# Kernel optimization log

Measured on AMD Instinct MI355X. Metric: run time of the kernel, lower is better.

Reference implementation:

```python
import jax, jax.numpy as jnp
import numpy as np

B, TQ, TK, D, DV = 8, 2048, 2048, 1024, 1024  # units == TK


def setup_inputs() -> dict:
    key = jax.random.key(0)
    kq, kk, kv, kb = jax.random.split(key, 4)
    q = jax.random.normal(kq, (B, TQ, D), dtype=jnp.float32)
    k = jax.random.normal(kk, (B, D, TK), dtype=jnp.float32)
    v = jax.random.normal(kv, (B, TK, DV), dtype=jnp.float32)
    b = 0.1 * jax.random.normal(kb, (TK,), dtype=jnp.float32)  # bias over key axis (units,)
    return {"q": q, "k": k, "v": v, "b": b}


def reference(q, k, v, b):
    # scores[b,i,j] = tanh(q_i . k_j + b_j)   -- additive-style biased dot scores
    scores = jnp.tanh(jnp.einsum("bqd,bdk->bqk", q, k) + b)  # [B, TQ, TK]
    # softmax over the key axis (axis=1 of the unbatched [TQ,TK] scores)
    weights = jax.nn.softmax(scores, axis=-1)
    # weighted sum of values
    context = jnp.einsum("bqk,bkv->bqv", weights, v)  # [B, TQ, DV]
    return context
```

## Files before the change

kernel.cpp:

```cpp
#include <hip/hip_runtime.h>
#include <hip/hip_bf16.h>
#include <stdint.h>

#define B_  8
#define TQ_ 2048
#define TK_ 2048
#define D_  1024
#define DV_ 1024

typedef __attribute__((ext_vector_type(8))) short  short8;
typedef __attribute__((ext_vector_type(4))) float  floatx4;

__device__ __forceinline__ void async_copy16(const void* g, void* l) {
  __builtin_amdgcn_global_load_lds(
      (const __attribute__((address_space(1))) unsigned int*)g,
      (__attribute__((address_space(3))) unsigned int*)l,
      16, 0, 0);
}

__device__ __forceinline__ ushort f2bf(float f) {
  union { __hip_bfloat16 b; ushort u; } cv;
  cv.b = __float2bfloat16(f);
  return cv.u;
}

__device__ __forceinline__ float bf2f(ushort u) {
  union { ushort u; __hip_bfloat16 b; } cv;
  cv.u = u;
  return __bfloat162float(cv.b);
}


__global__ void cvt_bf16(const float4* __restrict__ in, ushort4* __restrict__ out, int n4) {
  int i = blockIdx.x * 256 + threadIdx.x;
  if (i < n4) {
    float4 f = in[i];
    ushort4 o;
    o.x = f2bf(f.x); o.y = f2bf(f.y); o.z = f2bf(f.z); o.w = f2bf(f.w);
    out[i] = o;
  }
}

__global__ void transpose_cvt64(const float* __restrict__ in, ushort* __restrict__ out,
                                int R, int C) {
  __shared__ float tile[64][65];
  const int t  = threadIdx.x;
  const int c0 = blockIdx.x * 64, r0 = blockIdx.y * 64;
  const size_t z = (size_t)blockIdx.z * R * C;
  {
    const int row = t >> 4, col = (t & 15) * 4;
    #pragma unroll
    for (int ro = 0; ro < 4; ro++) {
      const float4 f = *(const float4*)&in[z + (size_t)(r0 + ro * 16 + row) * C + c0 + col];
      tile[ro * 16 + row][col + 0] = f.x;
      tile[ro * 16 + row][col + 1] = f.y;
      tile[ro * 16 + row][col + 2] = f.z;
      tile[ro * 16 + row][col + 3] = f.w;
    }
  }
  __syncthreads();
  {
    const int c = t >> 4, rg = (t & 15) * 4;
    #pragma unroll
    for (int ro = 0; ro < 4; ro++) {
      const int cc = ro * 16 + c;
      ushort4 o;
      o.x = f2bf(tile[rg + 0][cc]);
      o.y = f2bf(tile[rg + 1][cc]);
      o.z = f2bf(tile[rg + 2][cc]);
      o.w = f2bf(tile[rg + 3][cc]);
      *(ushort4*)&out[z + (size_t)(c0 + cc) * R + r0 + rg] = o;
    }
  }
}

template <int KDIM>
__device__ __forceinline__ void gemm_core(const ushort* __restrict__ Ab,
                                          const ushort* __restrict__ Bb,
                                          ushort* ldsA, ushort* ldsB,
                                          int bm0, int bn0,
                                          floatx4 (&acc)[4][4]) {
  const int t    = threadIdx.x;
  const int lane = t & 63;
  const int w    = t >> 6;
  const int wm   = w >> 1, wn = w & 1;
  const int lc   = lane & 15;
  const int q    = lane >> 4;

  const int achunk = (t & 3) ^ ((t >> 3) & 3);
  const char* ga0 = (const char*)(Ab + (size_t)(bm0 + (t >> 2)) * KDIM) + achunk * 16;
  const char* ga1 = ga0 + (size_t)64 * KDIM * 2;
  const char* gb0 = (const char*)(Bb + (size_t)(bn0 + (t >> 2)) * KDIM) + achunk * 16;
  const char* gb1 = gb0 + (size_t)64 * KDIM * 2;
  char* la0 = (char*)ldsA + t * 16;
  char* la1 = (char*)ldsA + 4096 + t * 16;
  char* lb0 = (char*)ldsB + t * 16;
  char* lb1 = (char*)ldsB + 4096 + t * 16;

  const int rA = wm * 64 + lc;
  const int rB = wn * 64 + lc;
  const int baseA = rA * 64 + (q ^ ((rA >> 1) & 3)) * 16;
  const int baseB = rB * 64 + (q ^ ((rB >> 1) & 3)) * 16;

  #pragma unroll
  for (int mi = 0; mi < 4; mi++)
    #pragma unroll
    for (int ni = 0; ni < 4; ni++)
      acc[mi][ni] = (floatx4){0.f, 0.f, 0.f, 0.f};

  for (int k0 = 0; k0 < KDIM; k0 += 32) {
    __syncthreads();
    async_copy16(ga0, la0);
    async_copy16(ga1, la1);
    async_copy16(gb0, lb0);
    async_copy16(gb1, lb1);
    ga0 += 64; ga1 += 64; gb0 += 64; gb1 += 64;
    __syncthreads();

    short8 af[4], bfr[4];
    #pragma unroll
    for (int i = 0; i < 4; i++) af[i]  = *(const short8*)((const char*)ldsA + baseA + i * 1024);
    #pragma unroll
    for (int i = 0; i < 4; i++) bfr[i] = *(const short8*)((const char*)ldsB + baseB + i * 1024);
    #pragma unroll
    for (int mi = 0; mi < 4; mi++)
      #pragma unroll
      for (int ni = 0; ni < 4; ni++)
        acc[mi][ni] = __builtin_amdgcn_mfma_f32_16x16x32_bf16(af[mi], bfr[ni],
                                                              acc[mi][ni], 0, 0, 0);
  }
}

__global__ void gemm_qk(const ushort* __restrict__ Q, const ushort* __restrict__ Kt,
                        const float* __restrict__ bias, ushort* __restrict__ P,
                        float* __restrict__ lsum) {
  __shared__ ushort ldsA[128 * 32];
  __shared__ ushort ldsB[128 * 32];
  const int z   = blockIdx.z;
  const int bm0 = blockIdx.y * 128;
  const int bn0 = blockIdx.x * 128;

  floatx4 acc[4][4];
  gemm_core<D_>(Q + (size_t)z * TQ_ * D_, Kt + (size_t)z * TK_ * D_,
                ldsA, ldsB, bm0, bn0, acc);

  const int lane = threadIdx.x & 63;
  const int w    = threadIdx.x >> 6;
  const int wm   = w >> 1, wn = w & 1;
  const int lc   = lane & 15;
  ushort* Pb = P + (size_t)z * TQ_ * TK_;
  float*  lz = lsum + z * TQ_;

  #pragma unroll
  for (int mi = 0; mi < 4; mi++) {
    int grow = bm0 + wm * 64 + mi * 16 + ((lane >> 4) << 2);
    float rs[4] = {0.f, 0.f, 0.f, 0.f};
    #pragma unroll
    for (int ni = 0; ni < 4; ni++) {
      int gcol = bn0 + wn * 64 + ni * 16 + lc;
      float bj = bias[gcol];
      #pragma unroll
      for (int r = 0; r < 4; r++) {
        float s = acc[mi][ni][r] + bj;
        float tnh = 1.f - 2.f / (__expf(2.f * s) + 1.f);
        float p   = __expf(tnh);
        ushort pu = f2bf(p);
        Pb[(size_t)(grow + r) * TK_ + gcol] = pu;
        rs[r] += bf2f(pu);
      }
    }
    #pragma unroll
    for (int r = 0; r < 4; r++) {
      rs[r] += __shfl_xor(rs[r], 1, 64);
      rs[r] += __shfl_xor(rs[r], 2, 64);
      rs[r] += __shfl_xor(rs[r], 4, 64);
      rs[r] += __shfl_xor(rs[r], 8, 64);
    }
    if (lc == 0) {
      #pragma unroll
      for (int r = 0; r < 4; r++) atomicAdd(&lz[grow + r], rs[r]);
    }
  }
}

__global__ void gemm_pv(const ushort* __restrict__ P, const ushort* __restrict__ Vt,
                        const float* __restrict__ lsum, float* __restrict__ out) {
  __shared__ ushort ldsA[128 * 32];
  __shared__ ushort ldsB[128 * 32];
  const int z   = blockIdx.z;
  const int bm0 = blockIdx.y * 128;
  const int bn0 = blockIdx.x * 128;

  floatx4 acc[4][4];
  gemm_core<TK_>(P + (size_t)z * TQ_ * TK_, Vt + (size_t)z * DV_ * TK_,
                 ldsA, ldsB, bm0, bn0, acc);

  const int lane = threadIdx.x & 63;
  const int w    = threadIdx.x >> 6;
  const int wm   = w >> 1, wn = w & 1;
  const int lc   = lane & 15;
  float* ob = out + (size_t)z * TQ_ * DV_;
  const float* lz = lsum + z * TQ_;

  #pragma unroll
  for (int mi = 0; mi < 4; mi++) {
    int grow = bm0 + wm * 64 + mi * 16 + ((lane >> 4) << 2);
    float linv[4];
    #pragma unroll
    for (int r = 0; r < 4; r++) linv[r] = 1.f / lz[grow + r];
    #pragma unroll
    for (int ni = 0; ni < 4; ni++) {
      int gcol = bn0 + wn * 64 + ni * 16 + lc;
      #pragma unroll
      for (int r = 0; r < 4; r++)
        ob[(size_t)(grow + r) * DV_ + gcol] = acc[mi][ni][r] * linv[r];
    }
  }
}


extern "C" void kernel_launch(void* const* d_in, const int* in_sizes, int n_in,
                              void* d_out, int out_size, void* d_ws, size_t ws_size,
                              hipStream_t stream) {
  const float* q    = (const float*)d_in[0];
  const float* k    = (const float*)d_in[1];
  const float* v    = (const float*)d_in[2];
  const float* bias = (const float*)d_in[3];
  float* out = (float*)d_out;

  char* ws = (char*)d_ws;
  ushort* qb   = (ushort*)(ws);
  ushort* ktb  = (ushort*)(ws + 33554432);
  ushort* vtb  = (ushort*)(ws + 67108864);
  ushort* P    = (ushort*)(ws + 100663296);
  float*  lsum = (float*)(ws + 167772160);

  hipMemsetAsync(lsum, 0, B_ * TQ_ * sizeof(float), stream);

  int n4q = B_ * TQ_ * D_ / 4;
  cvt_bf16<<<dim3(n4q / 256), dim3(256), 0, stream>>>((const float4*)q, (ushort4*)qb, n4q);
  transpose_cvt64<<<dim3(TK_ / 64, D_ / 64, B_), dim3(256), 0, stream>>>(k, ktb, D_, TK_);
  transpose_cvt64<<<dim3(DV_ / 64, TK_ / 64, B_), dim3(256), 0, stream>>>(v, vtb, TK_, DV_);

  gemm_qk<<<dim3(TK_ / 128, TQ_ / 128, B_), dim3(256), 0, stream>>>(qb, ktb, bias, P, lsum);
  gemm_pv<<<dim3(DV_ / 128, TQ_ / 128, B_), dim3(256), 0, stream>>>(P, vtb, lsum, out);
}
```

Baseline: 415.0 us.

## Double-buffer LDS tiles in GEMM core and fuse prep kernels into one launch

The shared GEMM core now uses two LDS buffers. The next K-slice's global-to-LDS async copy is issued right after the barrier, before the current slice is read from LDS and fed to MFMA, so each iteration needs one barrier instead of two and the load overlaps the math. The three conversion/transpose kernels for q, k and v are merged into a single prep launch that dispatches on blockIdx.z, which removes launch gaps. This doubles LDS use per block to 32KB, which may reduce occupancy.

```diff
diff --git a/kernel.cpp b/kernel.cpp
--- a/kernel.cpp
+++ b/kernel.cpp
@@ -31,27 +31,16 @@
 }
 
 
-__global__ void cvt_bf16(const float4* __restrict__ in, ushort4* __restrict__ out, int n4) {
-  int i = blockIdx.x * 256 + threadIdx.x;
-  if (i < n4) {
-    float4 f = in[i];
-    ushort4 o;
-    o.x = f2bf(f.x); o.y = f2bf(f.y); o.z = f2bf(f.z); o.w = f2bf(f.w);
-    out[i] = o;
-  }
-}
-
-__global__ void transpose_cvt64(const float* __restrict__ in, ushort* __restrict__ out,
-                                int R, int C) {
-  __shared__ float tile[64][65];
-  const int t  = threadIdx.x;
-  const int c0 = blockIdx.x * 64, r0 = blockIdx.y * 64;
-  const size_t z = (size_t)blockIdx.z * R * C;
+__device__ __forceinline__ void transpose_body(const float* __restrict__ in,
+                                               ushort* __restrict__ out,
+                                               int R, int C, int r0, int c0,
+                                               float (*tile)[65]) {
+  const int t = threadIdx.x;
   {
     const int row = t >> 4, col = (t & 15) * 4;
     #pragma unroll
     for (int ro = 0; ro < 4; ro++) {
-      const float4 f = *(const float4*)&in[z + (size_t)(r0 + ro * 16 + row) * C + c0 + col];
+      const float4 f = *(const float4*)&in[(size_t)(r0 + ro * 16 + row) * C + c0 + col];
       tile[ro * 16 + row][col + 0] = f.x;
       tile[ro * 16 + row][col + 1] = f.y;
       tile[ro * 16 + row][col + 2] = f.z;
@@ -69,8 +58,35 @@
       o.y = f2bf(tile[rg + 1][cc]);
       o.z = f2bf(tile[rg + 2][cc]);
       o.w = f2bf(tile[rg + 3][cc]);
-      *(ushort4*)&out[z + (size_t)(c0 + cc) * R + r0 + rg] = o;
-    }
+      *(ushort4*)&out[(size_t)(c0 + cc) * R + r0 + rg] = o;
+    }
+  }
+}
+
+__global__ void prep(const float* __restrict__ q, const float* __restrict__ k,
+                     const float* __restrict__ v, ushort* __restrict__ qb,
+                     ushort* __restrict__ ktb, ushort* __restrict__ vtb) {
+  __shared__ float tile[64][65];
+  const int task = blockIdx.z >> 3;
+  const int z    = blockIdx.z & 7;
+  if (task == 0) {
+    const float4* in  = (const float4*)(q + (size_t)z * TQ_ * D_);
+    ushort4*      oup = (ushort4*)(qb + (size_t)z * TQ_ * D_);
+    const int i0 = (blockIdx.y * 32 + blockIdx.x) * 1024 + threadIdx.x;
+    #pragma unroll
+    for (int it = 0; it < 4; it++) {
+      const int i = i0 + it * 256;
+      float4 f = in[i];
+      ushort4 o;
+      o.x = f2bf(f.x); o.y = f2bf(f.y); o.z = f2bf(f.z); o.w = f2bf(f.w);
+      oup[i] = o;
+    }
+  } else if (task == 1) {
+    transpose_body(k + (size_t)z * D_ * TK_, ktb + (size_t)z * TK_ * D_,
+                   D_, TK_, blockIdx.y * 64, blockIdx.x * 64, tile);
+  } else {
+    transpose_body(v + (size_t)z * TK_ * DV_, vtb + (size_t)z * DV_ * TK_,
+                   TK_, DV_, blockIdx.x * 64, blockIdx.y * 64, tile);
   }
 }
 
@@ -108,34 +124,46 @@
     for (int ni = 0; ni < 4; ni++)
       acc[mi][ni] = (floatx4){0.f, 0.f, 0.f, 0.f};
 
+  async_copy16(ga0, la0);
+  async_copy16(ga1, la1);
+  async_copy16(gb0, lb0);
+  async_copy16(gb1, lb1);
+  ga0 += 64; ga1 += 64; gb0 += 64; gb1 += 64;
+
+  int cur = 0;
   for (int k0 = 0; k0 < KDIM; k0 += 32) {
     __syncthreads();
-    async_copy16(ga0, la0);
-    async_copy16(ga1, la1);
-    async_copy16(gb0, lb0);
-    async_copy16(gb1, lb1);
-    ga0 += 64; ga1 += 64; gb0 += 64; gb1 += 64;
-    __syncthreads();
+    if (k0 + 32 < KDIM) {
+      const int nxt = cur ^ 8192;
+      async_copy16(ga0, la0 + nxt);
+      async_copy16(ga1, la1 + nxt);
+      async_copy16(gb0, lb0 + nxt);
+      async_copy16(gb1, lb1 + nxt);
+      ga0 += 64; ga1 += 64; gb0 += 64; gb1 += 64;
+    }
 
     short8 af[4], bfr[4];
     #pragma unroll
-    for (int i = 0; i < 4; i++) af[i]  = *(const short8*)((const char*)ldsA + baseA + i * 1024);
-    #pragma unroll
-    for (int i = 0; i < 4; i++) bfr[i] = *(const short8*)((const char*)ldsB + baseB + i * 1024);
+    for (int i = 0; i < 4; i++)
+      af[i]  = *(const short8*)((const char*)ldsA + cur + baseA + i * 1024);
+    #pragma unroll
+    for (int i = 0; i < 4; i++)
+      bfr[i] = *(const short8*)((const char*)ldsB + cur + baseB + i * 1024);
     #pragma unroll
     for (int mi = 0; mi < 4; mi++)
       #pragma unroll
       for (int ni = 0; ni < 4; ni++)
         acc[mi][ni] = __builtin_amdgcn_mfma_f32_16x16x32_bf16(af[mi], bfr[ni],
                                                               acc[mi][ni], 0, 0, 0);
+    cur ^= 8192;
   }
 }
 
 __global__ void gemm_qk(const ushort* __restrict__ Q, const ushort* __restrict__ Kt,
                         const float* __restrict__ bias, ushort* __restrict__ P,
                         float* __restrict__ lsum) {
-  __shared__ ushort ldsA[128 * 32];
-  __shared__ ushort ldsB[128 * 32];
+  __shared__ ushort ldsA[2 * 128 * 32];
+  __shared__ ushort ldsB[2 * 128 * 32];
   const int z   = blockIdx.z;
   const int bm0 = blockIdx.y * 128;
   const int bn0 = blockIdx.x * 128;
@@ -185,8 +213,8 @@
 
 __global__ void gemm_pv(const ushort* __restrict__ P, const ushort* __restrict__ Vt,
                         const float* __restrict__ lsum, float* __restrict__ out) {
-  __shared__ ushort ldsA[128 * 32];
-  __shared__ ushort ldsB[128 * 32];
+  __shared__ ushort ldsA[2 * 128 * 32];
+  __shared__ ushort ldsB[2 * 128 * 32];
   const int z   = blockIdx.z;
   const int bm0 = blockIdx.y * 128;
   const int bn0 = blockIdx.x * 128;
@@ -237,10 +265,7 @@
 
   hipMemsetAsync(lsum, 0, B_ * TQ_ * sizeof(float), stream);
 
-  int n4q = B_ * TQ_ * D_ / 4;
-  cvt_bf16<<<dim3(n4q / 256), dim3(256), 0, stream>>>((const float4*)q, (ushort4*)qb, n4q);
-  transpose_cvt64<<<dim3(TK_ / 64, D_ / 64, B_), dim3(256), 0, stream>>>(k, ktb, D_, TK_);
-  transpose_cvt64<<<dim3(DV_ / 64, TK_ / 64, B_), dim3(256), 0, stream>>>(v, vtb, TK_, DV_);
+  prep<<<dim3(32, 16, 24), dim3(256), 0, stream>>>(q, k, v, qb, ktb, vtb);
 
   gemm_qk<<<dim3(TK_ / 128, TQ_ / 128, B_), dim3(256), 0, stream>>>(qb, ktb, bias, P, lsum);
   gemm_pv<<<dim3(DV_ / 128, TQ_ / 128, B_), dim3(256), 0, stream>>>(P, vtb, lsum, out);
```

After: 411.3 us. Within noise of the previous version (-0.9%).
